# Performance work log

Hardware: AMD Instinct MI355X
Metric: run time of the kernel (lower is better)

The kernel has to match this reference:

```python
import jax, jax.numpy as jnp
import numpy as np

N, E, F_IN, OUT = 10000, 80000, 128, 32
H1, C1 = 8, 256   # conv1: heads=8, out_channels=256, concat=True
H2, C2 = 1, OUT   # conv2: heads=1, out_channels=OUT, concat=False
NEG_SLOPE = 0.2


def _add_self_loops(edge_index, edge_attr, n_nodes):
    # PyG fill_value='mean': self-loop edge_attr = mean of incoming edge attrs per dst node
    src, dst = edge_index[0], edge_index[1]
    s = jax.ops.segment_sum(edge_attr, dst, num_segments=n_nodes)
    cnt = jax.ops.segment_sum(jnp.ones((edge_attr.shape[0],), edge_attr.dtype), dst, num_segments=n_nodes)
    self_attr = s / jnp.maximum(cnt, 1.0)[:, None]
    loop = jnp.arange(n_nodes)
    return (jnp.concatenate([src, loop]), jnp.concatenate([dst, loop]),
            jnp.concatenate([edge_attr, self_attr], axis=0))


def _gatv2(x, src, dst, edge_attr, Wl, bl, Wr, br, We, att, bias, heads, out_ch, concat, n_nodes):
    xl = (x @ Wl + bl).reshape(n_nodes, heads, out_ch)   # source-side projection
    xr = (x @ Wr + br).reshape(n_nodes, heads, out_ch)   # target-side projection
    e = (edge_attr @ We).reshape(-1, heads, out_ch)      # edge feature projection (no bias in PyG)
    m = jax.nn.leaky_relu(xl[src] + xr[dst] + e, NEG_SLOPE)   # [Etot, H, C]
    logits = jnp.einsum('ehc,hc->eh', m, att)            # per-edge attention logits
    # segment softmax over edges grouped by destination node (stable)
    lmax = jax.ops.segment_max(logits, dst, num_segments=n_nodes)
    ex = jnp.exp(logits - lmax[dst])
    denom = jax.ops.segment_sum(ex, dst, num_segments=n_nodes)
    alpha = ex / denom[dst]                              # [Etot, H]
    out = jax.ops.segment_sum(xl[src] * alpha[:, :, None], dst, num_segments=n_nodes)  # [N, H, C]
    out = out.reshape(n_nodes, heads * out_ch) if concat else out.mean(axis=1)
    return out + bias


def setup_inputs() -> dict:
    key = jax.random.key(0)
    ks = jax.random.split(key, 17)
    s = 0.05
    return {
        'x': jax.random.normal(ks[0], (N, F_IN), jnp.float32),
        'edge_index': jax.random.randint(ks[1], (2, E), 0, N),
        'edge_attr': jax.random.normal(ks[2], (E, F_IN), jnp.float32),
        # conv1 params
        'Wl1': jax.random.normal(ks[3], (F_IN, H1 * C1), jnp.float32) * s,
        'bl1': jnp.zeros((H1 * C1,), jnp.float32),
        'Wr1': jax.random.normal(ks[4], (F_IN, H1 * C1), jnp.float32) * s,
        'br1': jnp.zeros((H1 * C1,), jnp.float32),
        'We1': jax.random.normal(ks[5], (F_IN, H1 * C1), jnp.float32) * s,
        'att1': jax.random.normal(ks[6], (H1, C1), jnp.float32) * s,
        'b1': jnp.zeros((H1 * C1,), jnp.float32),
        # conv2 params (input dim = H1*C1 = 2048)
        'Wl2': jax.random.normal(ks[7], (H1 * C1, H2 * C2), jnp.float32) * s,
        'bl2': jnp.zeros((H2 * C2,), jnp.float32),
        'Wr2': jax.random.normal(ks[8], (H1 * C1, H2 * C2), jnp.float32) * s,
        'br2': jnp.zeros((H2 * C2,), jnp.float32),
        'We2': jax.random.normal(ks[9], (F_IN, H2 * C2), jnp.float32) * s,
        'att2': jax.random.normal(ks[10], (H2, C2), jnp.float32) * s,
        'b2': jnp.zeros((C2,), jnp.float32),
    }


def reference(x, edge_index, edge_attr, Wl1, bl1, Wr1, br1, We1, att1, b1,
              Wl2, bl2, Wr2, br2, We2, att2, b2):
    # mode='eval': all dropouts are identity
    src, dst, ea = _add_self_loops(edge_index, edge_attr, N)
    h = _gatv2(x, src, dst, ea, Wl1, bl1, Wr1, br1, We1, att1, b1, H1, C1, True, N)
    h = jax.nn.relu(h)
    out = _gatv2(h, src, dst, ea, Wl2, bl2, Wr2, br2, We2, att2, b2, H2, C2, False, N)
    return jax.nn.relu(out)
```

## Files before the change

### kernel.cpp

```cpp
#include <hip/hip_runtime.h>
#include <hip/hip_bf16.h>

#define N_NODES 10000
#define N_EDGES 80000
#define ETOT (N_EDGES + N_NODES)
#define FD 128
#define D1 2048
#define D2 32
#define NEG 0.2f

typedef __hip_bfloat16 bf16;
typedef __attribute__((ext_vector_type(8))) short short8;
typedef __attribute__((ext_vector_type(4))) short short4v;
typedef __attribute__((ext_vector_type(4))) float f32x4;

__device__ __forceinline__ bf16 f2b(float v){ return __float2bfloat16(v); }
__device__ __forceinline__ short f2bs(float v){ bf16 t=__float2bfloat16(v); return *(short*)&t; }
__device__ __forceinline__ float b2fs(short s){
    return __uint_as_float(((unsigned int)(unsigned short)s) << 16);
}

__global__ void k_deg(const int* __restrict__ ei, int* __restrict__ deg){
    int e = blockIdx.x*256 + threadIdx.x;
    if(e < N_EDGES) atomicAdd(&deg[ei[N_EDGES+e]], 1);
}

__global__ void k_scan(const int* __restrict__ deg, int* __restrict__ row_start){
    __shared__ int sdata[256];
    int tid = threadIdx.x;
    const int CH = 40;
    int base = tid*CH;
    int lsum = 0;
    for(int i=0;i<CH;i++){ int v=base+i; if(v<N_NODES) lsum += deg[v]+1; }
    sdata[tid]=lsum; __syncthreads();
    for(int off=1; off<256; off<<=1){
        int val = (tid>=off)? sdata[tid-off] : 0;
        __syncthreads();
        sdata[tid] += val;
        __syncthreads();
    }
    int run = (tid>0)? sdata[tid-1] : 0;
    for(int i=0;i<CH;i++){
        int v=base+i;
        if(v<=N_NODES){
            row_start[v]=run;
            if(v<N_NODES) run += deg[v]+1;
        }
    }
}

__global__ void k_fill(const int* __restrict__ ei, const int* __restrict__ row_start,
                       int* __restrict__ cursor, int* __restrict__ ecsr,
                       int* __restrict__ srcs, int* __restrict__ dsts){
    int e = blockIdx.x*256 + threadIdx.x;
    if(e >= ETOT) return;
    int src = (e < N_EDGES) ? ei[e]          : (e - N_EDGES);
    int dst = (e < N_EDGES) ? ei[N_EDGES+e]  : (e - N_EDGES);
    int p = atomicAdd(&cursor[dst], 1);
    int pos = row_start[dst]+p;
    ecsr[pos] = e;
    srcs[pos] = src;
    dsts[pos] = dst;
}

__global__ void k_selfmean(const int* __restrict__ ecsr, const int* __restrict__ row_start,
                           const float* __restrict__ ea, float* __restrict__ self_attr){
    int v = blockIdx.x, t = threadIdx.x;
    int start=row_start[v], end=row_start[v+1];
    float s=0.f; int cnt=0;
    for(int i=start;i<end;i++){
        int e=ecsr[i];
        if(e<N_EDGES){ s += ea[(size_t)e*FD+t]; cnt++; }
    }
    self_attr[(size_t)v*FD+t] = s / fmaxf((float)cnt, 1.f);
}

__global__ void k_packW1(const float* __restrict__ W, short* __restrict__ Wb){
    int idx = blockIdx.x*256 + threadIdx.x;
    int k = idx >> 11, c = idx & 2047;
    int cb = c>>4, col = c&15, kc = k>>5, quad = (k>>3)&3, j = k&7;
    Wb[((size_t)(cb*4+kc)*64 + quad*16 + col)*8 + j] = f2bs(W[idx]);
}

__global__ void k_packW2(const float* __restrict__ Wl2, const float* __restrict__ Wr2,
                         short* __restrict__ Wb2){
    int idx = blockIdx.x*256 + threadIdx.x;
    int k = idx >> 6, c = idx & 63;
    float v = (c < 32) ? Wl2[k*32 + c] : Wr2[k*32 + (c-32)];
    int cb = c>>4, col = c&15, kc = k>>5, quad = (k>>3)&3, j = k&7;
    Wb2[((size_t)(cb*64+kc)*64 + quad*16 + col)*8 + j] = f2bs(v);
}

__global__ void k_packW2e(const float* __restrict__ We2, short* __restrict__ Wb2e){
    int idx = blockIdx.x*256 + threadIdx.x;
    int k = idx >> 5, c = idx & 31;
    int cb = c>>4, col = c&15, kc = k>>5, quad = (k>>3)&3, j = k&7;
    Wb2e[((size_t)(cb*4+kc)*64 + quad*16 + col)*8 + j] = f2bs(We2[idx]);
}

__global__ __launch_bounds__(256) void k_gemm1m(const float* __restrict__ x,
        const short* __restrict__ Wb, const float* __restrict__ bias,
        bf16* __restrict__ outp){
    __shared__ short a_lds[32*128];
    __shared__ float tile[4][32][20];
    int tid = threadIdx.x;
    int r0 = blockIdx.x*32;
    for(int q=tid; q<32*128; q+=256){
        int m=q>>7, k=q&127;
        int gr=r0+m;
        float v = (gr<N_NODES)? x[(size_t)gr*FD+k] : 0.f;
        int kc=k>>5, quad=(k>>3)&3, j=k&7;
        a_lds[((kc*4+quad)*32+m)*8+j] = f2bs(v);
    }
    __syncthreads();
    int w=tid>>6, lane=tid&63, quad=lane>>4, col=lane&15;
    int arow=lane&31, half=lane>>5;
    short8 af[2][4];
    #pragma unroll
    for(int mg=0;mg<2;mg++)
        #pragma unroll
        for(int kc=0;kc<4;kc++)
            af[mg][kc] = *(const short8*)&a_lds[((kc*4+quad)*32+mg*16+col)*8];
    int orow = r0 + arow;
    for(int cbl=0;cbl<32;cbl++){
        int cbg = w*32+cbl;
        f32x4 c0={0,0,0,0}, c1={0,0,0,0};
        #pragma unroll
        for(int kc=0;kc<4;kc++){
            short8 bfr = *(const short8*)(Wb + ((size_t)(cbg*4+kc)*64 + lane)*8);
            c0 = __builtin_amdgcn_mfma_f32_16x16x32_bf16(af[0][kc], bfr, c0, 0,0,0);
            c1 = __builtin_amdgcn_mfma_f32_16x16x32_bf16(af[1][kc], bfr, c1, 0,0,0);
        }
        #pragma unroll
        for(int rg=0;rg<4;rg++){
            tile[w][quad*4+rg][col]    = c0[rg];
            tile[w][16+quad*4+rg][col] = c1[rg];
        }
        int cg = cbg*16 + half*8;
        float4 t0 = *(float4*)&tile[w][arow][half*8];
        float4 t1 = *(float4*)&tile[w][arow][half*8+4];
        float4 b0 = *(const float4*)(bias+cg);
        float4 b1v = *(const float4*)(bias+cg+4);
        if(orow < N_NODES){
            float tv[8]={t0.x,t0.y,t0.z,t0.w,t1.x,t1.y,t1.z,t1.w};
            float bb[8]={b0.x,b0.y,b0.z,b0.w,b1v.x,b1v.y,b1v.z,b1v.w};
            short8 ov;
            #pragma unroll
            for(int j=0;j<8;j++) ov[j] = f2bs(tv[j]+bb[j]);
            *(short8*)(outp + (size_t)orow*D1 + cg) = ov;
        }
    }
}

__global__ __launch_bounds__(256) void k_logit1(const int* __restrict__ ecsr,
        const int* __restrict__ srcs, const int* __restrict__ dsts,
        const float* __restrict__ ea, const float* __restrict__ self_attr,
        const bf16* __restrict__ xl1, const bf16* __restrict__ xr1,
        const short* __restrict__ Wb, const short* __restrict__ Wb2e,
        const float* __restrict__ att1,
        float* __restrict__ logits1p, float* __restrict__ e2){
    __shared__ short a_lds[64*128];
    __shared__ float tile[4][32][20];
    __shared__ int ssrc[64], sdst[64], sed[64];
    int tid = threadIdx.x;
    int i0 = blockIdx.x*64;
    if(tid<64){
        int i=i0+tid; if(i>=ETOT) i=ETOT-1;
        sed[tid]=ecsr[i]; ssrc[tid]=srcs[i]; sdst[tid]=dsts[i];
    }
    __syncthreads();
    for(int q=tid; q<64*32; q+=256){
        int m=q>>5, kq=(q&31)*4;
        int e=sed[m];
        const float* sp = (e<N_EDGES)? (ea+(size_t)e*FD+kq) : (self_attr+(size_t)(e-N_EDGES)*FD+kq);
        float4 v4 = *(const float4*)sp;
        int kc=kq>>5, quad=(kq>>3)&3, j=kq&7;
        short4v sv; sv[0]=f2bs(v4.x); sv[1]=f2bs(v4.y); sv[2]=f2bs(v4.z); sv[3]=f2bs(v4.w);
        *(short4v*)&a_lds[((kc*4+quad)*64+m)*8+j] = sv;
    }
    __syncthreads();
    int w=tid>>6, lane=tid&63, quad=lane>>4, col=lane&15;
    int arow=lane&31, half=lane>>5;
    short8 af[4][4];
    #pragma unroll
    for(int mg=0;mg<4;mg++)
        #pragma unroll
        for(int kc=0;kc<4;kc++)
            af[mg][kc] = *(const short8*)&a_lds[((kc*4+quad)*64+mg*16+col)*8];
    const bf16* xlpA = xl1 + (size_t)ssrc[arow]*D1;
    const bf16* xrpA = xr1 + (size_t)sdst[arow]*D1;
    const bf16* xlpB = xl1 + (size_t)ssrc[32+arow]*D1;
    const bf16* xrpB = xr1 + (size_t)sdst[32+arow]*D1;
    float acch[4]={0.f,0.f,0.f,0.f};
    for(int cbl=0;cbl<32;cbl++){
        int cbg = w*32+cbl;
        f32x4 c0={0,0,0,0}, c1={0,0,0,0}, c2={0,0,0,0}, c3={0,0,0,0};
        #pragma unroll
        for(int kc=0;kc<4;kc++){
            short8 bfr = *(const short8*)(Wb + ((size_t)(cbg*4+kc)*64 + lane)*8);
            c0 = __builtin_amdgcn_mfma_f32_16x16x32_bf16(af[0][kc], bfr, c0, 0,0,0);
            c1 = __builtin_amdgcn_mfma_f32_16x16x32_bf16(af[1][kc], bfr, c1, 0,0,0);
            c2 = __builtin_amdgcn_mfma_f32_16x16x32_bf16(af[2][kc], bfr, c2, 0,0,0);
            c3 = __builtin_amdgcn_mfma_f32_16x16x32_bf16(af[3][kc], bfr, c3, 0,0,0);
        }
        int hs = cbl>>4;
        int cg = cbg*16 + half*8;
        float4 a0 = *(const float4*)(att1+cg);
        float4 a1 = *(const float4*)(att1+cg+4);
        float av[8]={a0.x,a0.y,a0.z,a0.w,a1.x,a1.y,a1.z,a1.w};
        #pragma unroll
        for(int rg=0;rg<4;rg++){
            tile[w][quad*4+rg][col]    = c0[rg];
            tile[w][16+quad*4+rg][col] = c1[rg];
        }
        {
            float4 t0 = *(float4*)&tile[w][arow][half*8];
            float4 t1 = *(float4*)&tile[w][arow][half*8+4];
            short8 xlv = *(const short8*)(xlpA + cg);
            short8 xrv = *(const short8*)(xrpA + cg);
            float tv[8]={t0.x,t0.y,t0.z,t0.w,t1.x,t1.y,t1.z,t1.w};
            float acc = acch[hs];
            #pragma unroll
            for(int j=0;j<8;j++){
                float m = tv[j] + b2fs(xlv[j]) + b2fs(xrv[j]);
                m = (m>0.f)? m : NEG*m;
                acc += av[j]*m;
            }
            acch[hs] = acc;
        }
        #pragma unroll
        for(int rg=0;rg<4;rg++){
            tile[w][quad*4+rg][col]    = c2[rg];
            tile[w][16+quad*4+rg][col] = c3[rg];
        }
        {
            float4 t0 = *(float4*)&tile[w][arow][half*8];
            float4 t1 = *(float4*)&tile[w][arow][half*8+4];
            short8 xlv = *(const short8*)(xlpB + cg);
            short8 xrv = *(const short8*)(xrpB + cg);
            float tv[8]={t0.x,t0.y,t0.z,t0.w,t1.x,t1.y,t1.z,t1.w};
            float acc = acch[2+hs];
            #pragma unroll
            for(int j=0;j<8;j++){
                float m = tv[j] + b2fs(xlv[j]) + b2fs(xrv[j]);
                m = (m>0.f)? m : NEG*m;
                acc += av[j]*m;
            }
            acch[2+hs] = acc;
        }
    }
    if(w<2){
        f32x4 c0={0,0,0,0}, c1={0,0,0,0}, c2={0,0,0,0}, c3={0,0,0,0};
        #pragma unroll
        for(int kc=0;kc<4;kc++){
            short8 bfr = *(const short8*)(Wb2e + ((size_t)(w*4+kc)*64 + lane)*8);
            c0 = __builtin_amdgcn_mfma_f32_16x16x32_bf16(af[0][kc], bfr, c0, 0,0,0);
            c1 = __builtin_amdgcn_mfma_f32_16x16x32_bf16(af[1][kc], bfr, c1, 0,0,0);
            c2 = __builtin_amdgcn_mfma_f32_16x16x32_bf16(af[2][kc], bfr, c2, 0,0,0);
            c3 = __builtin_amdgcn_mfma_f32_16x16x32_bf16(af[3][kc], bfr, c3, 0,0,0);
        }
        #pragma unroll
        for(int rg=0;rg<4;rg++){
            tile[w][quad*4+rg][col]    = c0[rg];
            tile[w][16+quad*4+rg][col] = c1[rg];
        }
        {
            int i=i0+arow;
            float4 t0 = *(float4*)&tile[w][arow][half*8];
            float4 t1 = *(float4*)&tile[w][arow][half*8+4];
            if(i<ETOT){
                *(float4*)(e2 + (size_t)i*32 + w*16 + half*8)     = t0;
                *(float4*)(e2 + (size_t)i*32 + w*16 + half*8 + 4) = t1;
            }
        }
        #pragma unroll
        for(int rg=0;rg<4;rg++){
            tile[w][quad*4+rg][col]    = c2[rg];
            tile[w][16+quad*4+rg][col] = c3[rg];
        }
        {
            int i=i0+32+arow;
            float4 t0 = *(float4*)&tile[w][arow][half*8];
            float4 t1 = *(float4*)&tile[w][arow][half*8+4];
            if(i<ETOT){
                *(float4*)(e2 + (size_t)i*32 + w*16 + half*8)     = t0;
                *(float4*)(e2 + (size_t)i*32 + w*16 + half*8 + 4) = t1;
            }
        }
    }
    #pragma unroll
    for(int r=0;r<4;r++) acch[r] += __shfl_xor(acch[r],32);
    if(lane<32){
        int iA=i0+arow;
        if(iA<ETOT){
            logits1p[(size_t)iA*8 + w*2  ] = acch[0];
            logits1p[(size_t)iA*8 + w*2+1] = acch[1];
        }
        int iB=i0+32+arow;
        if(iB<ETOT){
            logits1p[(size_t)iB*8 + w*2  ] = acch[2];
            logits1p[(size_t)iB*8 + w*2+1] = acch[3];
        }
    }
}

__global__ void k_agg1(const int* __restrict__ srcs, const int* __restrict__ row_start,
                       const float* __restrict__ logits1p, const bf16* __restrict__ xl1,
                       const float* __restrict__ b1, bf16* __restrict__ hb){
    __shared__ float dden[8];
    __shared__ float salpha[32][8];
    int tid=threadIdx.x, v=blockIdx.x;
    int start=row_start[v], end=row_start[v+1];
    if(tid<8) dden[tid]=0.f;
    __syncthreads();
    float ds[8]={0,0,0,0,0,0,0,0};
    for(int i=start+tid;i<end;i+=256){
        const float* lp = logits1p+(size_t)i*8;
        float4 l0=*(const float4*)lp, l1=*(const float4*)(lp+4);
        ds[0]+=__expf(l0.x); ds[1]+=__expf(l0.y); ds[2]+=__expf(l0.z); ds[3]+=__expf(l0.w);
        ds[4]+=__expf(l1.x); ds[5]+=__expf(l1.y); ds[6]+=__expf(l1.z); ds[7]+=__expf(l1.w);
    }
    #pragma unroll
    for(int j=0;j<8;j++){
        float val=ds[j];
        #pragma unroll
        for(int off=32;off>=1;off>>=1) val += __shfl_down(val,off);
        if((tid&63)==0) atomicAdd(&dden[j], val);
    }
    __syncthreads();
    float rden[8];
    #pragma unroll
    for(int j=0;j<8;j++) rden[j]=1.f/dden[j];
    int myc = tid*8;
    int hj  = tid>>5;
    float acc[8]={0,0,0,0,0,0,0,0};
    for(int base=start; base<end; base+=32){
        int nle = end-base; if(nle>32) nle=32;
        __syncthreads();
        if(tid < nle*8){
            int le=tid>>3, j=tid&7;
            salpha[le][j] = __expf(logits1p[(size_t)(base+le)*8+j])*rden[j];
        }
        __syncthreads();
        for(int le=0; le<nle; le++){
            int src=srcs[base+le];
            short8 xv = *(const short8*)(xl1 + (size_t)src*D1 + myc);
            float al = salpha[le][hj];
            #pragma unroll
            for(int j=0;j<8;j++) acc[j] += al*b2fs(xv[j]);
        }
    }
    float4 bb0=*(const float4*)(b1+myc), bb1=*(const float4*)(b1+myc+4);
    float bv[8]={bb0.x,bb0.y,bb0.z,bb0.w,bb1.x,bb1.y,bb1.z,bb1.w};
    short8 ov;
    #pragma unroll
    for(int j=0;j<8;j++) ov[j] = f2bs(fmaxf(acc[j]+bv[j],0.f));
    *(short8*)(hb + (size_t)v*D1 + myc) = ov;
}

__global__ __launch_bounds__(256) void k_gemm2(const bf16* __restrict__ hb,
        const short* __restrict__ Wb2, const float* __restrict__ bl2,
        const float* __restrict__ br2, float* __restrict__ xl2, float* __restrict__ xr2){
    __shared__ float cacc[4][16][64];
    int tid=threadIdx.x, w=tid>>6, lane=tid&63, quad=lane>>4, col=lane&15;
    int r0 = blockIdx.x*16;
    const bf16* hp = hb + (size_t)(r0+col)*D1 + quad*8;
    f32x4 acc[4] = {{0,0,0,0},{0,0,0,0},{0,0,0,0},{0,0,0,0}};
    for(int kc=w*16; kc<w*16+16; kc++){
        short8 af = *(const short8*)(hp + kc*32);
        #pragma unroll
        for(int cb=0;cb<4;cb++){
            short8 bfr = *(const short8*)(Wb2 + ((size_t)(cb*64+kc)*64 + lane)*8);
            acc[cb] = __builtin_amdgcn_mfma_f32_16x16x32_bf16(af, bfr, acc[cb], 0,0,0);
        }
    }
    #pragma unroll
    for(int cb=0;cb<4;cb++)
        #pragma unroll
        for(int rg=0;rg<4;rg++)
            cacc[w][quad*4+rg][cb*16+col] = acc[cb][rg];
    __syncthreads();
    #pragma unroll
    for(int i=0;i<4;i++){
        int idx = tid + 256*i;
        int r = idx>>6, c = idx&63;
        float s = cacc[0][r][c]+cacc[1][r][c]+cacc[2][r][c]+cacc[3][r][c];
        int rr = r0 + r;
        if(c<32) xl2[rr*32+c]      = s + bl2[c];
        else     xr2[rr*32+(c-32)] = s + br2[c-32];
    }
}

__global__ void k_logit2(const int* __restrict__ srcs, const int* __restrict__ dsts,
                         const float* __restrict__ e2,
                         const float* __restrict__ xl2, const float* __restrict__ xr2,
                         const float* __restrict__ att2, float* __restrict__ logits2p){
    int tid=threadIdx.x, i0=blockIdx.x*8;
    int le=tid>>5, c=tid&31;
    int i=i0+le; if(i>=ETOT) i=ETOT-1;
    int src=srcs[i], dst=dsts[i];
    float m = e2[(size_t)i*32+c] + xl2[src*32+c] + xr2[dst*32+c];
    m = (m>0.f)? m : NEG*m;
    float p = att2[c]*m;
    #pragma unroll
    for(int off=16;off>=1;off>>=1) p += __shfl_down(p,off,32);
    if(c==0 && i0+le<ETOT) logits2p[i]=p;
}

__global__ void k_agg2(const int* __restrict__ srcs, const int* __restrict__ row_start,
                       const float* __restrict__ logits2p, const float* __restrict__ xl2,
                       const float* __restrict__ b2v, float* __restrict__ out){
    int tid=threadIdx.x, v=blockIdx.x;
    int start=row_start[v], end=row_start[v+1];
    float ds=0.f;
    for(int i=start+tid;i<end;i+=64) ds += __expf(logits2p[i]);
    #pragma unroll
    for(int off=32;off>=1;off>>=1) ds += __shfl_xor(ds,off);
    float rden = 1.f/ds;
    int half=tid>>5, c=tid&31;
    float acc=0.f;
    for(int i=start+half;i<end;i+=2){
        int src=srcs[i];
        acc += __expf(logits2p[i])*rden * xl2[src*32+c];
    }
    acc += __shfl_xor(acc,32);
    if(tid<32){
        float o = acc + b2v[c];
        out[(size_t)v*D2+c] = fmaxf(o,0.f);
    }
}

extern "C" void kernel_launch(void* const* d_in, const int* in_sizes, int n_in,
                              void* d_out, int out_size, void* d_ws, size_t ws_size,
                              hipStream_t stream) {
    const float* x    = (const float*)d_in[0];
    const int*   ei   = (const int*)d_in[1];
    const float* ea   = (const float*)d_in[2];
    const float* Wl1  = (const float*)d_in[3];
    const float* bl1  = (const float*)d_in[4];
    const float* Wr1  = (const float*)d_in[5];
    const float* br1  = (const float*)d_in[6];
    const float* We1  = (const float*)d_in[7];
    const float* att1 = (const float*)d_in[8];
    const float* b1   = (const float*)d_in[9];
    const float* Wl2  = (const float*)d_in[10];
    const float* bl2  = (const float*)d_in[11];
    const float* Wr2  = (const float*)d_in[12];
    const float* br2  = (const float*)d_in[13];
    const float* We2  = (const float*)d_in[14];
    const float* att2 = (const float*)d_in[15];
    const float* b2v  = (const float*)d_in[16];
    float* out = (float*)d_out;

    char* ws = (char*)d_ws;
    size_t off = 0;
    auto alloc = [&](size_t bytes)->char* {
        char* p = ws + off;
        off += (bytes + 255) & ~(size_t)255;
        return p;
    };
    float* self_attr = (float*)alloc((size_t)N_NODES*FD*4);
    int*   deg       = (int*)  alloc((size_t)N_NODES*4);
    int*   cursor    = (int*)  alloc((size_t)N_NODES*4);
    int*   row_start = (int*)  alloc((size_t)(N_NODES+1)*4);
    int*   ecsr      = (int*)  alloc((size_t)ETOT*4);
    int*   srcs      = (int*)  alloc((size_t)ETOT*4);
    int*   dsts      = (int*)  alloc((size_t)ETOT*4);
    float* logits1p  = (float*)alloc((size_t)ETOT*8*4);
    float* logits2p  = (float*)alloc((size_t)ETOT*4);
    float* e2        = (float*)alloc((size_t)ETOT*32*4);
    bf16*  xl1       = (bf16*) alloc((size_t)N_NODES*D1*2);
    bf16*  xr1       = (bf16*) alloc((size_t)N_NODES*D1*2);
    bf16*  hb        = (bf16*) alloc((size_t)N_NODES*D1*2);
    float* xl2       = (float*)alloc((size_t)N_NODES*D2*4);
    float* xr2       = (float*)alloc((size_t)N_NODES*D2*4);
    short* Wb1       = (short*)alloc((size_t)FD*D1*2);
    short* Wbl1      = (short*)alloc((size_t)FD*D1*2);
    short* Wbr1      = (short*)alloc((size_t)FD*D1*2);
    short* Wb2       = (short*)alloc((size_t)D1*64*2);
    short* Wb2e      = (short*)alloc((size_t)FD*D2*2);
    (void)ws_size; (void)in_sizes; (void)n_in; (void)out_size;

    hipMemsetAsync(deg,    0, (size_t)N_NODES*4, stream);
    hipMemsetAsync(cursor, 0, (size_t)N_NODES*4, stream);

    k_deg<<<(N_EDGES+255)/256, 256, 0, stream>>>(ei, deg);
    k_scan<<<1, 256, 0, stream>>>(deg, row_start);
    k_fill<<<(ETOT+255)/256, 256, 0, stream>>>(ei, row_start, cursor, ecsr, srcs, dsts);
    k_selfmean<<<N_NODES, 128, 0, stream>>>(ecsr, row_start, ea, self_attr);
    k_packW1<<<(FD*D1)/256, 256, 0, stream>>>(We1, Wb1);
    k_packW1<<<(FD*D1)/256, 256, 0, stream>>>(Wl1, Wbl1);
    k_packW1<<<(FD*D1)/256, 256, 0, stream>>>(Wr1, Wbr1);
    k_packW2<<<(D1*64)/256, 256, 0, stream>>>(Wl2, Wr2, Wb2);
    k_packW2e<<<(FD*D2)/256, 256, 0, stream>>>(We2, Wb2e);

    k_gemm1m<<<(N_NODES+31)/32, 256, 0, stream>>>(x, Wbl1, bl1, xl1);
    k_gemm1m<<<(N_NODES+31)/32, 256, 0, stream>>>(x, Wbr1, br1, xr1);

    k_logit1<<<(ETOT+63)/64, 256, 0, stream>>>(ecsr, srcs, dsts, ea, self_attr,
                                               xl1, xr1, Wb1, Wb2e, att1, logits1p, e2);
    k_agg1<<<N_NODES, 256, 0, stream>>>(srcs, row_start, logits1p, xl1, b1, hb);

    k_gemm2<<<N_NODES/16, 256, 0, stream>>>(hb, Wb2, bl2, br2, xl2, xr2);
    k_logit2<<<(ETOT+7)/8, 256, 0, stream>>>(srcs, dsts, e2, xl2, xr2, att2, logits2p);
    k_agg2<<<N_NODES, 64, 0, stream>>>(srcs, row_start, logits2p, xl2, b2v, out);
}
```

Measured before the change: 487.3 us.

## Swap MFMA operand roles in edge logit kernel to drop LDS transpose

The edge-feature projection MFMA in the conv1 logit kernel now uses the weights as the A operand and the edge tile as B. Each lane then holds four consecutive channels for one edge directly in registers, so the per-wave LDS tile staging and transpose round-trip is removed. The epilogue gathers 4-wide xl/xr slices per edge and reduces logits with two cross-lane shuffles instead of one. The trade-off is narrower gather loads (8 bytes instead of 16) and more shuffles.

```diff
diff --git a/kernel.cpp b/kernel.cpp
--- a/kernel.cpp
+++ b/kernel.cpp
@@ -159,8 +159,7 @@
         const short* __restrict__ Wb, const short* __restrict__ Wb2e,
         const float* __restrict__ att1,
         float* __restrict__ logits1p, float* __restrict__ e2){
-    __shared__ short a_lds[64*128];
-    __shared__ float tile[4][32][20];
+    __shared__ short b_lds[64*128];
     __shared__ int ssrc[64], sdst[64], sed[64];
     int tid = threadIdx.x;
     int i0 = blockIdx.x*64;
@@ -176,132 +175,85 @@
         float4 v4 = *(const float4*)sp;
         int kc=kq>>5, quad=(kq>>3)&3, j=kq&7;
         short4v sv; sv[0]=f2bs(v4.x); sv[1]=f2bs(v4.y); sv[2]=f2bs(v4.z); sv[3]=f2bs(v4.w);
-        *(short4v*)&a_lds[((kc*4+quad)*64+m)*8+j] = sv;
-    }
-    __syncthreads();
-    int w=tid>>6, lane=tid&63, quad=lane>>4, col=lane&15;
-    int arow=lane&31, half=lane>>5;
-    short8 af[4][4];
-    #pragma unroll
-    for(int mg=0;mg<4;mg++)
+        *(short4v*)&b_lds[((kc*4+quad)*64+m)*8+j] = sv;
+    }
+    __syncthreads();
+    int w=tid>>6, lane=tid&63, quad=lane>>4, nn=lane&15;
+    short8 bea[4][4];
+    #pragma unroll
+    for(int g=0;g<4;g++)
         #pragma unroll
         for(int kc=0;kc<4;kc++)
-            af[mg][kc] = *(const short8*)&a_lds[((kc*4+quad)*64+mg*16+col)*8];
-    const bf16* xlpA = xl1 + (size_t)ssrc[arow]*D1;
-    const bf16* xrpA = xr1 + (size_t)sdst[arow]*D1;
-    const bf16* xlpB = xl1 + (size_t)ssrc[32+arow]*D1;
-    const bf16* xrpB = xr1 + (size_t)sdst[32+arow]*D1;
-    float acch[4]={0.f,0.f,0.f,0.f};
+            bea[g][kc] = *(const short8*)&b_lds[((kc*4+quad)*64 + g*16 + nn)*8];
+    int esrc[4], edst[4];
+    #pragma unroll
+    for(int g=0;g<4;g++){ esrc[g]=ssrc[g*16+nn]; edst[g]=sdst[g*16+nn]; }
+    float acc[4][2]={{0,0},{0,0},{0,0},{0,0}};
     for(int cbl=0;cbl<32;cbl++){
         int cbg = w*32+cbl;
+        int cg4 = cbg*16 + quad*4;
+        short8 aw[4];
+        #pragma unroll
+        for(int kc=0;kc<4;kc++)
+            aw[kc] = *(const short8*)(Wb + ((size_t)(cbg*4+kc)*64 + lane)*8);
         f32x4 c0={0,0,0,0}, c1={0,0,0,0}, c2={0,0,0,0}, c3={0,0,0,0};
         #pragma unroll
         for(int kc=0;kc<4;kc++){
-            short8 bfr = *(const short8*)(Wb + ((size_t)(cbg*4+kc)*64 + lane)*8);
-            c0 = __builtin_amdgcn_mfma_f32_16x16x32_bf16(af[0][kc], bfr, c0, 0,0,0);
-            c1 = __builtin_amdgcn_mfma_f32_16x16x32_bf16(af[1][kc], bfr, c1, 0,0,0);
-            c2 = __builtin_amdgcn_mfma_f32_16x16x32_bf16(af[2][kc], bfr, c2, 0,0,0);
-            c3 = __builtin_amdgcn_mfma_f32_16x16x32_bf16(af[3][kc], bfr, c3, 0,0,0);
-        }
+            c0 = __builtin_amdgcn_mfma_f32_16x16x32_bf16(aw[kc], bea[0][kc], c0, 0,0,0);
+            c1 = __builtin_amdgcn_mfma_f32_16x16x32_bf16(aw[kc], bea[1][kc], c1, 0,0,0);
+            c2 = __builtin_amdgcn_mfma_f32_16x16x32_bf16(aw[kc], bea[2][kc], c2, 0,0,0);
+            c3 = __builtin_amdgcn_mfma_f32_16x16x32_bf16(aw[kc], bea[3][kc], c3, 0,0,0);
+        }
+        float4 av = *(const float4*)(att1 + cg4);
+        float avv[4]={av.x,av.y,av.z,av.w};
         int hs = cbl>>4;
-        int cg = cbg*16 + half*8;
-        float4 a0 = *(const float4*)(att1+cg);
-        float4 a1 = *(const float4*)(att1+cg+4);
-        float av[8]={a0.x,a0.y,a0.z,a0.w,a1.x,a1.y,a1.z,a1.w};
-        #pragma unroll
-        for(int rg=0;rg<4;rg++){
-            tile[w][quad*4+rg][col]    = c0[rg];
-            tile[w][16+quad*4+rg][col] = c1[rg];
-        }
-        {
-            float4 t0 = *(float4*)&tile[w][arow][half*8];
-            float4 t1 = *(float4*)&tile[w][arow][half*8+4];
-            short8 xlv = *(const short8*)(xlpA + cg);
-            short8 xrv = *(const short8*)(xrpA + cg);
-            float tv[8]={t0.x,t0.y,t0.z,t0.w,t1.x,t1.y,t1.z,t1.w};
-            float acc = acch[hs];
+        f32x4 cc[4]={c0,c1,c2,c3};
+        #pragma unroll
+        for(int g=0;g<4;g++){
+            short4v xl4 = *(const short4v*)(xl1 + (size_t)esrc[g]*D1 + cg4);
+            short4v xr4 = *(const short4v*)(xr1 + (size_t)edst[g]*D1 + cg4);
+            float a = acc[g][hs];
             #pragma unroll
-            for(int j=0;j<8;j++){
-                float m = tv[j] + b2fs(xlv[j]) + b2fs(xrv[j]);
-                m = (m>0.f)? m : NEG*m;
-                acc += av[j]*m;
+            for(int rg=0;rg<4;rg++){
+                float m = cc[g][rg] + b2fs(xl4[rg]) + b2fs(xr4[rg]);
+                m = fmaxf(m, NEG*m);
+                a += avv[rg]*m;
             }
-            acch[hs] = acc;
-        }
-        #pragma unroll
-        for(int rg=0;rg<4;rg++){
-            tile[w][quad*4+rg][col]    = c2[rg];
-            tile[w][16+quad*4+rg][col] = c3[rg];
-        }
-        {
-            float4 t0 = *(float4*)&tile[w][arow][half*8];
-            float4 t1 = *(float4*)&tile[w][arow][half*8+4];
-            short8 xlv = *(const short8*)(xlpB + cg);
-            short8 xrv = *(const short8*)(xrpB + cg);
-            float tv[8]={t0.x,t0.y,t0.z,t0.w,t1.x,t1.y,t1.z,t1.w};
-            float acc = acch[2+hs];
-            #pragma unroll
-            for(int j=0;j<8;j++){
-                float m = tv[j] + b2fs(xlv[j]) + b2fs(xrv[j]);
-                m = (m>0.f)? m : NEG*m;
-                acc += av[j]*m;
-            }
-            acch[2+hs] = acc;
+            acc[g][hs] = a;
         }
     }
     if(w<2){
         f32x4 c0={0,0,0,0}, c1={0,0,0,0}, c2={0,0,0,0}, c3={0,0,0,0};
         #pragma unroll
         for(int kc=0;kc<4;kc++){
-            short8 bfr = *(const short8*)(Wb2e + ((size_t)(w*4+kc)*64 + lane)*8);
-            c0 = __builtin_amdgcn_mfma_f32_16x16x32_bf16(af[0][kc], bfr, c0, 0,0,0);
-            c1 = __builtin_amdgcn_mfma_f32_16x16x32_bf16(af[1][kc], bfr, c1, 0,0,0);
-            c2 = __builtin_amdgcn_mfma_f32_16x16x32_bf16(af[2][kc], bfr, c2, 0,0,0);
-            c3 = __builtin_amdgcn_mfma_f32_16x16x32_bf16(af[3][kc], bfr, c3, 0,0,0);
-        }
-        #pragma unroll
-        for(int rg=0;rg<4;rg++){
-            tile[w][quad*4+rg][col]    = c0[rg];
-            tile[w][16+quad*4+rg][col] = c1[rg];
-        }
-        {
-            int i=i0+arow;
-            float4 t0 = *(float4*)&tile[w][arow][half*8];
-            float4 t1 = *(float4*)&tile[w][arow][half*8+4];
+            short8 aw2 = *(const short8*)(Wb2e + ((size_t)(w*4+kc)*64 + lane)*8);
+            c0 = __builtin_amdgcn_mfma_f32_16x16x32_bf16(aw2, bea[0][kc], c0, 0,0,0);
+            c1 = __builtin_amdgcn_mfma_f32_16x16x32_bf16(aw2, bea[1][kc], c1, 0,0,0);
+            c2 = __builtin_amdgcn_mfma_f32_16x16x32_bf16(aw2, bea[2][kc], c2, 0,0,0);
+            c3 = __builtin_amdgcn_mfma_f32_16x16x32_bf16(aw2, bea[3][kc], c3, 0,0,0);
+        }
+        f32x4 cc[4]={c0,c1,c2,c3};
+        #pragma unroll
+        for(int g=0;g<4;g++){
+            int i = i0 + g*16 + nn;
             if(i<ETOT){
-                *(float4*)(e2 + (size_t)i*32 + w*16 + half*8)     = t0;
-                *(float4*)(e2 + (size_t)i*32 + w*16 + half*8 + 4) = t1;
+                float4 t={cc[g][0],cc[g][1],cc[g][2],cc[g][3]};
+                *(float4*)(e2 + (size_t)i*32 + w*16 + quad*4) = t;
             }
         }
-        #pragma unroll
-        for(int rg=0;rg<4;rg++){
-            tile[w][quad*4+rg][col]    = c2[rg];
-            tile[w][16+quad*4+rg][col] = c3[rg];
-        }
-        {
-            int i=i0+32+arow;
-            float4 t0 = *(float4*)&tile[w][arow][half*8];
-            float4 t1 = *(float4*)&tile[w][arow][half*8+4];
-            if(i<ETOT){
-                *(float4*)(e2 + (size_t)i*32 + w*16 + half*8)     = t0;
-                *(float4*)(e2 + (size_t)i*32 + w*16 + half*8 + 4) = t1;
+    }
+    #pragma unroll
+    for(int g=0;g<4;g++)
+        #pragma unroll
+        for(int h=0;h<2;h++){
+            float v=acc[g][h];
+            v += __shfl_xor(v,16);
+            v += __shfl_xor(v,32);
+            if(lane<16){
+                int i=i0+g*16+lane;
+                if(i<ETOT) logits1p[(size_t)i*8 + w*2+h] = v;
             }
         }
-    }
-    #pragma unroll
-    for(int r=0;r<4;r++) acch[r] += __shfl_xor(acch[r],32);
-    if(lane<32){
-        int iA=i0+arow;
-        if(iA<ETOT){
-            logits1p[(size_t)iA*8 + w*2  ] = acch[0];
-            logits1p[(size_t)iA*8 + w*2+1] = acch[1];
-        }
-        int iB=i0+32+arow;
-        if(iB<ETOT){
-            logits1p[(size_t)iB*8 + w*2  ] = acch[2];
-            logits1p[(size_t)iB*8 + w*2+1] = acch[3];
-        }
-    }
 }
 
 __global__ void k_agg1(const int* __restrict__ srcs, const int* __restrict__ row_start,
```

After: 545.5 us. 1.12x slower.
